# Kernel optimization log

Hardware: AMD Instinct MI355X
Metric: run time of the kernel (lower is better)

Reference implementation:

```python
import jax, jax.numpy as jnp
import numpy as np

N, E, MUL = 50000, 400000, 32
SQ3 = float(np.sqrt(3.0))


def setup_inputs() -> dict:
    key = jax.random.key(0)
    ks = jax.random.split(key, 16)
    rn = lambda k, s: jax.random.normal(k, s, dtype=jnp.float32)
    return {
        "x": rn(ks[0], (N, 4 * MUL)),                       # 32x0e + 32x1o
        "node_attr": jnp.ones((N, 1), jnp.float32),          # 1x0e
        "edge_src": jax.random.randint(ks[1], (E,), 0, N),
        "edge_dst": jax.random.randint(ks[2], (E,), 0, N),
        "edge_sh": rn(ks[3], (E, 4)),                        # SH(lmax=1): 0e + 1o
        "edge_scalars": jax.random.uniform(ks[4], (E, 10), dtype=jnp.float32),
        "W_fc1": rn(ks[5], (10, 100)),
        "W_fc2": rn(ks[6], (100, 4 * MUL)),
        "W_sc0": rn(ks[7], (MUL, MUL)),
        "W_sc1": rn(ks[8], (MUL, MUL)),
        "W_l1_0": rn(ks[9], (MUL, MUL)),
        "W_l1_1": rn(ks[10], (MUL, MUL)),
        "W_l2_0": rn(ks[11], (2 * MUL, MUL)),
        "W_l2_1": rn(ks[12], (2 * MUL, MUL)),
        "W_alpha": rn(ks[13], (2 * MUL, 1)),
    }


def reference(x, node_attr, edge_src, edge_dst, edge_sh, edge_scalars,
              W_fc1, W_fc2, W_sc0, W_sc1, W_l1_0, W_l1_1, W_l2_0, W_l2_1, W_alpha):
    n = x.shape[0]
    x0 = x[:, :MUL]                       # [N, 32]  scalars (0e)
    x1 = x[:, MUL:].reshape(n, MUL, 3)    # [N, 32, 3] vectors (1o)
    a = node_attr                          # [N, 1]
    inv = 1.0 / np.sqrt(MUL)
    inv2 = 1.0 / np.sqrt(2 * MUL)

    # self-connection FCTP(x, attr) -> out irreps (attr is scalar -> per-l linear)
    sc0 = (x0 @ W_sc0) * inv * a
    sc1 = jnp.einsum('nuc,uv->nvc', x1, W_sc1) * inv * a[:, :, None]
    sc = jnp.concatenate([sc0, sc1.reshape(n, 3 * MUL)], axis=1)

    # lin1
    y0 = (x0 @ W_l1_0) * inv * a
    y1 = jnp.einsum('nuc,uv->nvc', x1, W_l1_1) * inv * a[:, :, None]

    # radial MLP -> per-edge tensor-product weights (4 uvu paths x MUL)
    h = jax.nn.silu(edge_scalars @ W_fc1 / np.sqrt(10.0))
    w = (h @ W_fc2) / np.sqrt(100.0)      # [E, 4*MUL]
    w00, w11 = w[:, :MUL], w[:, MUL:2 * MUL]
    w01, w10 = w[:, 2 * MUL:3 * MUL], w[:, 3 * MUL:]

    # gather at source nodes
    x0e = y0[edge_src]                    # [E, 32]
    x1e = y1[edge_src]                    # [E, 32, 3]
    sh0 = edge_sh[:, :1]                  # [E, 1]
    sh1 = edge_sh[:, 1:4]                 # [E, 3]

    # CG-structured 'uvu' paths
    m00 = w00 * x0e * sh0                                           # 0e x 0e -> 0e
    m11 = w11 * jnp.einsum('euc,ec->eu', x1e, sh1) / SQ3            # 1o x 1o -> 0e
    m01 = w01[:, :, None] * x0e[:, :, None] * sh1[:, None, :]       # 0e x 1o -> 1o
    m10 = w10[:, :, None] * x1e * sh0[:, :, None]                   # 1o x 0e -> 1o
    edge_feat = jnp.concatenate(
        [m00, m11, m01.reshape(-1, 3 * MUL), m10.reshape(-1, 3 * MUL)], axis=1)  # [E, 256]

    # scatter-mean to destination nodes
    sums = jax.ops.segment_sum(edge_feat, edge_dst, num_segments=n)
    cnt = jax.ops.segment_sum(jnp.ones((edge_feat.shape[0],), x.dtype), edge_dst, num_segments=n)
    mean = sums / jnp.maximum(cnt, 1.0)[:, None]                    # [N, 256]

    mid0 = mean[:, :2 * MUL]                                        # 64x0e
    mid1 = mean[:, 2 * MUL:].reshape(n, 2 * MUL, 3)                 # 64x1o

    alpha = (mid0 @ W_alpha) * inv2 * a                             # [N, 1]
    c0 = (mid0 @ W_l2_0) * inv2 * a
    c1 = jnp.einsum('nuc,uv->nvc', mid1, W_l2_1) * inv2 * a[:, :, None]
    conv = jnp.concatenate([c0, c1.reshape(n, 3 * MUL)], axis=1)

    # output mask of sc is all ones here -> alpha gating as in source
    return sc + alpha * conv
```

## Files before the change

kernel.cpp:

```cpp
#include <hip/hip_runtime.h>
#include <hip/hip_bf16.h>

#define MUL 32
#define SCAN_CH 1024

typedef _Float16 f16x8 __attribute__((ext_vector_type(8)));
typedef float f32x4 __attribute__((ext_vector_type(4)));

static __device__ __forceinline__ float silu_f(float z) {
    return z / (1.0f + __expf(-z));
}

__global__ __launch_bounds__(256) void node_pre_kernel(
    const float* __restrict__ x, const float* __restrict__ attr,
    const float* __restrict__ Wsc0, const float* __restrict__ Wsc1,
    const float* __restrict__ Wl10, const float* __restrict__ Wl11,
    float* __restrict__ sc_out, _Float16* __restrict__ y_out, int N)
{
    __shared__ float sX[4][128];
    const int tid = threadIdx.x;
    const int wid = tid >> 6, L = tid & 63;
    float* xs = sX[wid];
    const float inv = 0.17677669529663687f;

    const bool t0 = (L < 32);
    const int i1 = t0 ? 0 : (L - 32);
    const int v1 = i1 / 3, c1 = i1 - v1 * 3;
    const int i2 = L + 32;
    const int v2 = i2 / 3, c2 = i2 - v2 * 3;

    const int xb1 = t0 ? 0 : (32 + c1);
    const int xst1 = t0 ? 1 : 3;

    float wA[32], wB[32], wC[32], wD[32];
#pragma unroll
    for (int u = 0; u < 32; ++u) {
        wA[u] = t0 ? Wsc0[u * 32 + L] : Wsc1[u * 32 + v1];
        wB[u] = t0 ? Wl10[u * 32 + L] : Wl11[u * 32 + v1];
        wC[u] = Wsc1[u * 32 + v2];
        wD[u] = Wl11[u * 32 + v2];
    }

    const int stride = gridDim.x * 4;
    for (int n = blockIdx.x * 4 + wid; n < N; n += stride) {
        xs[L]      = x[(size_t)n * 128 + L];
        xs[64 + L] = x[(size_t)n * 128 + 64 + L];
        const float scale = inv * attr[n];
        float a0 = 0.f, a1 = 0.f, b0 = 0.f, b1 = 0.f;
#pragma unroll
        for (int u = 0; u < 32; ++u) {
            const float xv1 = xs[xb1 + u * xst1];
            const float xv2 = xs[32 + u * 3 + c2];
            a0 += xv1 * wA[u];
            a1 += xv1 * wB[u];
            b0 += xv2 * wC[u];
            b1 += xv2 * wD[u];
        }
        sc_out[(size_t)n * 128 + L]      = a0 * scale;
        sc_out[(size_t)n * 128 + 64 + L] = b0 * scale;
        y_out [(size_t)n * 128 + L]      = (_Float16)(a1 * scale);
        y_out [(size_t)n * 128 + 64 + L] = (_Float16)(b1 * scale);
    }
}

__global__ void hist_kernel(const int* __restrict__ edst, int* __restrict__ deg, int E)
{
    int i = blockIdx.x * blockDim.x + threadIdx.x;
    const int stride = gridDim.x * blockDim.x;
    for (; i < E; i += stride) atomicAdd(&deg[edst[i]], 1);
}

__global__ __launch_bounds__(256) void scanA_kernel(
    const int* __restrict__ deg, int* __restrict__ bsum, int N)
{
    __shared__ int red[256];
    const int t = threadIdx.x, b = blockIdx.x;
    const int base = b * SCAN_CH;
    int s = 0;
#pragma unroll
    for (int k = 0; k < 4; ++k) {
        const int idx = base + t + k * 256;
        if (idx < N) s += deg[idx];
    }
    red[t] = s;
    __syncthreads();
    for (int off = 128; off; off >>= 1) {
        if (t < off) red[t] += red[t + off];
        __syncthreads();
    }
    if (t == 0) bsum[b] = red[0];
}

__global__ __launch_bounds__(256) void scanB_kernel(
    const int* __restrict__ bsum, int* __restrict__ boff, int NB)
{
    __shared__ int s[256];
    const int t = threadIdx.x;
    const int v = (t < NB) ? bsum[t] : 0;
    s[t] = v;
    __syncthreads();
    for (int off = 1; off < 256; off <<= 1) {
        const int add = (t >= off) ? s[t - off] : 0;
        __syncthreads();
        s[t] += add;
        __syncthreads();
    }
    if (t < NB) boff[t] = s[t] - v;
}

__global__ __launch_bounds__(256) void scanC_kernel(
    const int* __restrict__ deg, const int* __restrict__ boff,
    int* __restrict__ row_ptr, int N)
{
    __shared__ int ts[256];
    const int t = threadIdx.x, b = blockIdx.x;
    const int base = b * SCAN_CH + t * 4;
    int d0 = 0, d1 = 0, d2 = 0, d3 = 0;
    if (base + 0 < N) d0 = deg[base + 0];
    if (base + 1 < N) d1 = deg[base + 1];
    if (base + 2 < N) d2 = deg[base + 2];
    if (base + 3 < N) d3 = deg[base + 3];
    const int tsum = d0 + d1 + d2 + d3;
    ts[t] = tsum;
    __syncthreads();
    for (int off = 1; off < 256; off <<= 1) {
        const int add = (t >= off) ? ts[t - off] : 0;
        __syncthreads();
        ts[t] += add;
        __syncthreads();
    }
    int run = boff[b] + ts[t] - tsum;
    if (base + 0 <= N) row_ptr[base + 0] = run;
    run += d0;
    if (base + 1 <= N) row_ptr[base + 1] = run;
    run += d1;
    if (base + 2 <= N) row_ptr[base + 2] = run;
    run += d2;
    if (base + 3 <= N) row_ptr[base + 3] = run;
}

__global__ void fill_kernel(
    const int* __restrict__ esrc, const int* __restrict__ edst,
    const float* __restrict__ esh,
    const int* __restrict__ row_ptr, int* __restrict__ cur,
    int* __restrict__ csr2edge, int* __restrict__ src_s, float4* __restrict__ sh_s,
    int E)
{
    int i = blockIdx.x * blockDim.x + threadIdx.x;
    const int stride = gridDim.x * blockDim.x;
    for (; i < E; i += stride) {
        const int d = edst[i];
        const int p = row_ptr[d] + atomicAdd(&cur[d], 1);
        csr2edge[p] = i;
        src_s[p] = esrc[i];
        sh_s[p] = *(const float4*)&esh[(size_t)i * 4];
    }
}

__global__ __launch_bounds__(512) void edge_w_kernel(
    const float* __restrict__ escal, const int* __restrict__ csr2edge,
    const float* __restrict__ Wfc1, const float* __restrict__ Wfc2,
    _Float16* __restrict__ w_s, int E)
{
    __shared__ _Float16 sW2T[128 * 128];
    __shared__ _Float16 sH[8][16 * 128];

    const int tid = threadIdx.x;
    const int wid = tid >> 6;
    const int l   = tid & 63;
    const int c16 = l & 15;
    const int kq  = l >> 4;

    _Float16* Hw = sH[wid];

    {
        int* z2 = (int*)sW2T;
        for (int i = tid; i < 128 * 128 / 2; i += 512) z2[i] = 0;
    }
    __syncthreads();
    for (int i = tid; i < 100 * 128; i += 512) {
        const int k = i >> 7, col = i & 127;
        sW2T[col * 128 + (k ^ ((col & 7) << 3))] = (_Float16)Wfc2[i];
    }

    f16x8 bW1[7];
#pragma unroll
    for (int cb = 0; cb < 7; ++cb) {
        const int col = cb * 16 + c16;
#pragma unroll
        for (int j = 0; j < 8; ++j) {
            const int k = kq * 8 + j;
            bW1[cb][j] = (k < 10 && col < 100) ? (_Float16)Wfc1[k * 100 + col]
                                               : (_Float16)0.f;
        }
    }
#pragma unroll
    for (int r = 0; r < 4; ++r) {
        const int row = kq * 4 + r;
        const int col = 112 + c16;
        Hw[row * 128 + (col ^ ((row & 7) << 3))] = (_Float16)0.f;
    }
    __syncthreads();

    const float inv_s10 = 0.31622776601683794f;

    const int gw = blockIdx.x * 8 + wid;
    const int nw = gridDim.x * 8;
    const int step = nw * 16;

    int base = gw * 16;
    f16x8 a1;
    {
        const int ge = base + c16;
        const int ee = (ge < E) ? csr2edge[ge] : 0;
#pragma unroll
        for (int j = 0; j < 8; ++j) {
            const int k = kq * 8 + j;
            a1[j] = (k < 10 && ge < E) ? (_Float16)escal[(size_t)ee * 10 + k]
                                       : (_Float16)0.f;
        }
    }

    for (; base < E; base += step) {
#pragma unroll
        for (int cb = 0; cb < 7; ++cb) {
            f32x4 z = {0.f, 0.f, 0.f, 0.f};
            z = __builtin_amdgcn_mfma_f32_16x16x32_f16(a1, bW1[cb], z, 0, 0, 0);
#pragma unroll
            for (int r = 0; r < 4; ++r) {
                const int row = kq * 4 + r;
                const int col = cb * 16 + c16;
                const float h = silu_f(z[r] * inv_s10) * 0.1f;
                Hw[row * 128 + (col ^ ((row & 7) << 3))] = (_Float16)h;
            }
        }

        f16x8 a1n;
        {
            const int ge = base + step + c16;
            const int ee = (ge < E) ? csr2edge[ge] : 0;
#pragma unroll
            for (int j = 0; j < 8; ++j) {
                const int k = kq * 8 + j;
                a1n[j] = (k < 10 && ge < E)
                         ? (_Float16)escal[(size_t)ee * 10 + k]
                         : (_Float16)0.f;
            }
        }

        f32x4 acc0 = {0.f,0.f,0.f,0.f}, acc1 = {0.f,0.f,0.f,0.f};
        f32x4 acc2 = {0.f,0.f,0.f,0.f}, acc3 = {0.f,0.f,0.f,0.f};
        f32x4 acc4 = {0.f,0.f,0.f,0.f}, acc5 = {0.f,0.f,0.f,0.f};
        f32x4 acc6 = {0.f,0.f,0.f,0.f}, acc7 = {0.f,0.f,0.f,0.f};
#pragma unroll
        for (int kk = 0; kk < 4; ++kk) {
            const f16x8 a2 = *(const f16x8*)&Hw[c16 * 128 +
                                ((kk * 32 + kq * 8) ^ ((c16 & 7) << 3))];
#define BFRAG(CB) (*(const f16x8*)&sW2T[((CB) * 16 + c16) * 128 + \
                       ((kk * 32 + kq * 8) ^ ((c16 & 7) << 3))])
            acc0 = __builtin_amdgcn_mfma_f32_16x16x32_f16(a2, BFRAG(0), acc0, 0, 0, 0);
            acc1 = __builtin_amdgcn_mfma_f32_16x16x32_f16(a2, BFRAG(1), acc1, 0, 0, 0);
            acc2 = __builtin_amdgcn_mfma_f32_16x16x32_f16(a2, BFRAG(2), acc2, 0, 0, 0);
            acc3 = __builtin_amdgcn_mfma_f32_16x16x32_f16(a2, BFRAG(3), acc3, 0, 0, 0);
            acc4 = __builtin_amdgcn_mfma_f32_16x16x32_f16(a2, BFRAG(4), acc4, 0, 0, 0);
            acc5 = __builtin_amdgcn_mfma_f32_16x16x32_f16(a2, BFRAG(5), acc5, 0, 0, 0);
            acc6 = __builtin_amdgcn_mfma_f32_16x16x32_f16(a2, BFRAG(6), acc6, 0, 0, 0);
            acc7 = __builtin_amdgcn_mfma_f32_16x16x32_f16(a2, BFRAG(7), acc7, 0, 0, 0);
#undef BFRAG
        }

#define STAGE_CB(CB, ACC)                                                     \
        {                                                                     \
            _Pragma("unroll")                                                 \
            for (int r = 0; r < 4; ++r) {                                     \
                const int row = kq * 4 + r;                                   \
                const int col = (CB) * 16 + c16;                              \
                Hw[row * 128 + (col ^ ((row & 7) << 3))] = (_Float16)(ACC)[r];\
            }                                                                 \
        }
        STAGE_CB(0, acc0) STAGE_CB(1, acc1) STAGE_CB(2, acc2) STAGE_CB(3, acc3)
        STAGE_CB(4, acc4) STAGE_CB(5, acc5) STAGE_CB(6, acc6) STAGE_CB(7, acc7)
#undef STAGE_CB

#pragma unroll
        for (int i = 0; i < 4; ++i) {
            const int e = i * 4 + (l >> 4);
            const int colb = (l & 15) * 8;
            const f16x8 v = *(const f16x8*)&Hw[e * 128 +
                                (colb ^ ((e & 7) << 3))];
            if (base + e < E)
                *(f16x8*)&w_s[(size_t)(base + e) * 128 + colb] = v;
        }

        a1 = a1n;
    }
}

__global__ __launch_bounds__(256) void gather_post_kernel(
    const _Float16* __restrict__ w_s, const int* __restrict__ src_s,
    const float4* __restrict__ sh_s, const int* __restrict__ row_ptr,
    const _Float16* __restrict__ y, const float* __restrict__ attr,
    const float* __restrict__ Wl20, const float* __restrict__ Wl21,
    const float* __restrict__ Walpha,
    float* __restrict__ out, int N)
{
    __shared__ float sW0T[32 * 68];
    __shared__ float sW1T[32 * 68];
    __shared__ float sWa[64];
    __shared__ float sMid[4][256];

    const int tid = threadIdx.x;
    for (int i = tid; i < 64 * 32; i += 256) {
        const int u = i >> 5, o = i & 31;
        sW0T[o * 68 + u] = Wl20[i];
        sW1T[o * 68 + u] = Wl21[i];
    }
    if (tid < 64) sWa[tid] = Walpha[tid];
    __syncthreads();

    const int wid = tid >> 6;
    const int L   = tid & 63;
    const bool hi = (L >= 32);
    const int u   = L & 31;

    const int wAi = hi ? 32 + u : u;
    const int wBi = hi ? 96 + u : 64 + u;
    const int yi0 = hi ? 32 + 3 * u + 0 : u;
    const int yi1 = hi ? 32 + 3 * u + 1 : u;
    const int yi2 = hi ? 32 + 3 * u + 2 : u;
    const float mulA = hi ? 0.5773502691896258f : 1.0f;

    const int o1m = L - 32;
    const int v1 = hi ? o1m / 3 : 0;
    const int c1 = hi ? o1m - v1 * 3 : 0;
    const int o2m = L + 32;
    const int v2 = o2m / 3;
    const int c2 = o2m - v2 * 3;
    const float* wrow1 = hi ? (sW1T + v1 * 68) : (sW0T + L * 68);
    const float* wrow2 = sW1T + v2 * 68;

    float* midw = &sMid[wid][0];
    const float* msrc1c = hi ? (midw + 64 + c1 * 64) : midw;
    const float* msrc2c = midw + 64 + c2 * 64;

#define ACC_EDGE(sh, wAv, wBv, q0, q1, q2) do {                        \
        const float sA0 = hi ? (sh).y : (sh).x;                        \
        const float sA1 = hi ? (sh).z : 0.f;                           \
        const float sA2 = hi ? (sh).w : 0.f;                           \
        const float b1s = hi ? (sh).x : (sh).y;                        \
        const float b2s = hi ? (sh).x : (sh).z;                        \
        const float b3s = hi ? (sh).x : (sh).w;                        \
        accA += (wAv) * mulA * ((q0) * sA0 + (q1) * sA1 + (q2) * sA2); \
        acc1 += (wBv) * (q0) * b1s;                                    \
        acc2 += (wBv) * (q1) * b2s;                                    \
        acc3 += (wBv) * (q2) * b3s;                                    \
    } while (0)

    const int waves_glob = gridDim.x * 4;
    for (int n = blockIdx.x * 4 + wid; n < N; n += waves_glob) {
        const int jlo = row_ptr[n];
        const int jhi = row_ptr[n + 1];
        const int deg = jhi - jlo;
        if (deg <= 0) continue;

        float accA = 0.f, acc1 = 0.f, acc2 = 0.f, acc3 = 0.f;

        int j = jlo;
        for (; j + 2 <= jhi; j += 2) {
            const int sa = src_s[j];
            const int sb = src_s[j + 1];
            const float4 shA = sh_s[j];
            const float4 shB = sh_s[j + 1];
            const _Float16* wra = w_s + (size_t)j * 128;
            const _Float16* wrb = wra + 128;
            const _Float16* yra = y + (size_t)sa * 128;
            const _Float16* yrb = y + (size_t)sb * 128;
            const float wAa = (float)wra[wAi], wBa = (float)wra[wBi];
            const float qa0 = (float)yra[yi0], qa1 = (float)yra[yi1], qa2 = (float)yra[yi2];
            const float wAb = (float)wrb[wAi], wBb = (float)wrb[wBi];
            const float qb0 = (float)yrb[yi0], qb1 = (float)yrb[yi1], qb2 = (float)yrb[yi2];
            ACC_EDGE(shA, wAa, wBa, qa0, qa1, qa2);
            ACC_EDGE(shB, wAb, wBb, qb0, qb1, qb2);
        }
        if (j < jhi) {
            const int sa = src_s[j];
            const float4 shA = sh_s[j];
            const _Float16* wra = w_s + (size_t)j * 128;
            const _Float16* yra = y + (size_t)sa * 128;
            const float wAa = (float)wra[wAi], wBa = (float)wra[wBi];
            const float qa0 = (float)yra[yi0], qa1 = (float)yra[yi1], qa2 = (float)yra[yi2];
            ACC_EDGE(shA, wAa, wBa, qa0, qa1, qa2);
        }

        const float rdeg = 1.0f / (float)deg;
        const float a = attr[n];

        float term = accA * rdeg * sWa[L];
#pragma unroll
        for (int off = 32; off; off >>= 1) term += __shfl_xor(term, off);
        const float alpha = term * 0.125f * a;

        midw[L]            = accA * rdeg;
        midw[64 + L]       = acc1 * rdeg;
        midw[128 + L]      = acc2 * rdeg;
        midw[192 + L]      = acc3 * rdeg;

        float cv1 = 0.f, cv2 = 0.f;
#pragma unroll
        for (int kk = 0; kk < 16; ++kk) {
            const float4 m1 = *(const float4*)&msrc1c[4 * kk];
            const float4 m2 = *(const float4*)&msrc2c[4 * kk];
            const float4 w1 = *(const float4*)&wrow1[4 * kk];
            const float4 w2 = *(const float4*)&wrow2[4 * kk];
            cv1 += m1.x * w1.x + m1.y * w1.y + m1.z * w1.z + m1.w * w1.w;
            cv2 += m2.x * w2.x + m2.y * w2.y + m2.z * w2.z + m2.w * w2.w;
        }
        const float f = alpha * 0.125f * a;
        const size_t ob = (size_t)n * 128;
        out[ob + L]      += f * cv1;
        out[ob + 64 + L] += f * cv2;
    }
#undef ACC_EDGE
}

extern "C" void kernel_launch(void* const* d_in, const int* in_sizes, int n_in,
                              void* d_out, int out_size, void* d_ws, size_t ws_size,
                              hipStream_t stream)
{
    const float* x      = (const float*)d_in[0];
    const float* attr   = (const float*)d_in[1];
    const int*   esrc   = (const int*)  d_in[2];
    const int*   edst   = (const int*)  d_in[3];
    const float* esh    = (const float*)d_in[4];
    const float* escal  = (const float*)d_in[5];
    const float* Wfc1   = (const float*)d_in[6];
    const float* Wfc2   = (const float*)d_in[7];
    const float* Wsc0   = (const float*)d_in[8];
    const float* Wsc1   = (const float*)d_in[9];
    const float* Wl10   = (const float*)d_in[10];
    const float* Wl11   = (const float*)d_in[11];
    const float* Wl20   = (const float*)d_in[12];
    const float* Wl21   = (const float*)d_in[13];
    const float* Walpha = (const float*)d_in[14];

    const int N = in_sizes[1];
    const int E = in_sizes[2];
    float* out = (float*)d_out;

    char* p = (char*)d_ws;
    _Float16* y   = (_Float16*)p; p += (size_t)N * 128 * sizeof(_Float16);
    int* row_ptr  = (int*)p;      p += (size_t)(N + 1) * sizeof(int);
    int* deg      = (int*)p;      p += (size_t)N * sizeof(int);
    int* cur      = (int*)p;      p += (size_t)N * sizeof(int);
    int* bsum     = (int*)p;      p += 256 * sizeof(int);
    int* boff     = (int*)p;      p += 256 * sizeof(int);
    int* csr2edge = (int*)p;      p += (size_t)E * sizeof(int);
    int* src_s    = (int*)p;      p += (size_t)E * sizeof(int);
    p = (char*)(((uintptr_t)p + 15) & ~(uintptr_t)15);
    float4* sh_s  = (float4*)p;   p += (size_t)E * sizeof(float4);
    _Float16* w_s = (_Float16*)p;

    const int NB = (N + SCAN_CH) / SCAN_CH;

    hipMemsetAsync(deg, 0, (size_t)2 * N * sizeof(int), stream);

    node_pre_kernel<<<1024, 256, 0, stream>>>(x, attr, Wsc0, Wsc1, Wl10, Wl11,
                                              out, y, N);
    hist_kernel<<<512, 256, 0, stream>>>(edst, deg, E);
    scanA_kernel<<<NB, 256, 0, stream>>>(deg, bsum, N);
    scanB_kernel<<<1, 256, 0, stream>>>(bsum, boff, NB);
    scanC_kernel<<<NB, 256, 0, stream>>>(deg, boff, row_ptr, N);
    fill_kernel<<<512, 256, 0, stream>>>(esrc, edst, esh, row_ptr, cur,
                                         csr2edge, src_s, sh_s, E);
    edge_w_kernel<<<512, 512, 0, stream>>>(escal, csr2edge, Wfc1, Wfc2, w_s, E);
    gather_post_kernel<<<4096, 256, 0, stream>>>(w_s, src_s, sh_s, row_ptr,
                                                 y, attr, Wl20, Wl21, Walpha,
                                                 out, N);
}
```

Measured before the change: 237.0 us.

## Double-buffer per-wave H tile in edge weight MLP and halve block size

Restructures the edge radial-MLP kernel so each wave keeps two LDS H buffers and runs a software pipeline: the second GEMM and store of the current tile are followed by the first GEMM plus SiLU of the next tile, with escal loads prefetched two steps ahead. The block shrinks from 8 waves to 4 to keep LDS use the same, which halves the total number of waves in the 512-block grid. This aims to overlap MFMA, LDS traffic and global loads within a wave, but fewer waves means less latency hiding across waves.

```diff
diff --git a/kernel.cpp b/kernel.cpp
--- a/kernel.cpp
+++ b/kernel.cpp
@@ -157,13 +157,13 @@
     }
 }
 
-__global__ __launch_bounds__(512) void edge_w_kernel(
+__global__ __launch_bounds__(256) void edge_w_kernel(
     const float* __restrict__ escal, const int* __restrict__ csr2edge,
     const float* __restrict__ Wfc1, const float* __restrict__ Wfc2,
     _Float16* __restrict__ w_s, int E)
 {
     __shared__ _Float16 sW2T[128 * 128];
-    __shared__ _Float16 sH[8][16 * 128];
+    __shared__ _Float16 sH[4][2][16 * 128];
 
     const int tid = threadIdx.x;
     const int wid = tid >> 6;
@@ -171,14 +171,15 @@
     const int c16 = l & 15;
     const int kq  = l >> 4;
 
-    _Float16* Hw = sH[wid];
+    _Float16* Hw0 = sH[wid][0];
+    _Float16* Hw1 = sH[wid][1];
 
     {
         int* z2 = (int*)sW2T;
-        for (int i = tid; i < 128 * 128 / 2; i += 512) z2[i] = 0;
-    }
-    __syncthreads();
-    for (int i = tid; i < 100 * 128; i += 512) {
+        for (int i = tid; i < 128 * 128 / 2; i += 256) z2[i] = 0;
+    }
+    __syncthreads();
+    for (int i = tid; i < 100 * 128; i += 256) {
         const int k = i >> 7, col = i & 127;
         sW2T[col * 128 + (k ^ ((col & 7) << 3))] = (_Float16)Wfc2[i];
     }
@@ -198,102 +199,118 @@
     for (int r = 0; r < 4; ++r) {
         const int row = kq * 4 + r;
         const int col = 112 + c16;
-        Hw[row * 128 + (col ^ ((row & 7) << 3))] = (_Float16)0.f;
+        Hw0[row * 128 + (col ^ ((row & 7) << 3))] = (_Float16)0.f;
+        Hw1[row * 128 + (col ^ ((row & 7) << 3))] = (_Float16)0.f;
     }
     __syncthreads();
 
     const float inv_s10 = 0.31622776601683794f;
 
-    const int gw = blockIdx.x * 8 + wid;
-    const int nw = gridDim.x * 8;
+    const int gw = blockIdx.x * 4 + wid;
+    const int nw = gridDim.x * 4;
     const int step = nw * 16;
 
-    int base = gw * 16;
-    f16x8 a1;
-    {
-        const int ge = base + c16;
-        const int ee = (ge < E) ? csr2edge[ge] : 0;
-#pragma unroll
-        for (int j = 0; j < 8; ++j) {
-            const int k = kq * 8 + j;
-            a1[j] = (k < 10 && ge < E) ? (_Float16)escal[(size_t)ee * 10 + k]
-                                       : (_Float16)0.f;
-        }
-    }
-
-    for (; base < E; base += step) {
-#pragma unroll
-        for (int cb = 0; cb < 7; ++cb) {
-            f32x4 z = {0.f, 0.f, 0.f, 0.f};
-            z = __builtin_amdgcn_mfma_f32_16x16x32_f16(a1, bW1[cb], z, 0, 0, 0);
-#pragma unroll
-            for (int r = 0; r < 4; ++r) {
-                const int row = kq * 4 + r;
-                const int col = cb * 16 + c16;
-                const float h = silu_f(z[r] * inv_s10) * 0.1f;
-                Hw[row * 128 + (col ^ ((row & 7) << 3))] = (_Float16)h;
-            }
-        }
-
-        f16x8 a1n;
-        {
-            const int ge = base + step + c16;
-            const int ee = (ge < E) ? csr2edge[ge] : 0;
-#pragma unroll
-            for (int j = 0; j < 8; ++j) {
-                const int k = kq * 8 + j;
-                a1n[j] = (k < 10 && ge < E)
-                         ? (_Float16)escal[(size_t)ee * 10 + k]
-                         : (_Float16)0.f;
-            }
-        }
-
-        f32x4 acc0 = {0.f,0.f,0.f,0.f}, acc1 = {0.f,0.f,0.f,0.f};
-        f32x4 acc2 = {0.f,0.f,0.f,0.f}, acc3 = {0.f,0.f,0.f,0.f};
-        f32x4 acc4 = {0.f,0.f,0.f,0.f}, acc5 = {0.f,0.f,0.f,0.f};
-        f32x4 acc6 = {0.f,0.f,0.f,0.f}, acc7 = {0.f,0.f,0.f,0.f};
-#pragma unroll
-        for (int kk = 0; kk < 4; ++kk) {
-            const f16x8 a2 = *(const f16x8*)&Hw[c16 * 128 +
-                                ((kk * 32 + kq * 8) ^ ((c16 & 7) << 3))];
-#define BFRAG(CB) (*(const f16x8*)&sW2T[((CB) * 16 + c16) * 128 + \
-                       ((kk * 32 + kq * 8) ^ ((c16 & 7) << 3))])
-            acc0 = __builtin_amdgcn_mfma_f32_16x16x32_f16(a2, BFRAG(0), acc0, 0, 0, 0);
-            acc1 = __builtin_amdgcn_mfma_f32_16x16x32_f16(a2, BFRAG(1), acc1, 0, 0, 0);
-            acc2 = __builtin_amdgcn_mfma_f32_16x16x32_f16(a2, BFRAG(2), acc2, 0, 0, 0);
-            acc3 = __builtin_amdgcn_mfma_f32_16x16x32_f16(a2, BFRAG(3), acc3, 0, 0, 0);
-            acc4 = __builtin_amdgcn_mfma_f32_16x16x32_f16(a2, BFRAG(4), acc4, 0, 0, 0);
-            acc5 = __builtin_amdgcn_mfma_f32_16x16x32_f16(a2, BFRAG(5), acc5, 0, 0, 0);
-            acc6 = __builtin_amdgcn_mfma_f32_16x16x32_f16(a2, BFRAG(6), acc6, 0, 0, 0);
-            acc7 = __builtin_amdgcn_mfma_f32_16x16x32_f16(a2, BFRAG(7), acc7, 0, 0, 0);
-#undef BFRAG
-        }
-
-#define STAGE_CB(CB, ACC)                                                     \
+#define LOAD_A1(DST, B)                                                       \
+    {                                                                         \
+        const int ge_ = (B) + c16;                                            \
+        const int ee_ = (ge_ < E) ? csr2edge[ge_] : 0;                        \
+        _Pragma("unroll")                                                     \
+        for (int j_ = 0; j_ < 8; ++j_) {                                      \
+            const int k_ = kq * 8 + j_;                                       \
+            (DST)[j_] = (k_ < 10 && ge_ < E)                                  \
+                        ? (_Float16)escal[(size_t)ee_ * 10 + k_]              \
+                        : (_Float16)0.f;                                      \
+        }                                                                     \
+    }
+
+#define PHASE1(A1, H)                                                         \
+    {                                                                         \
+        _Pragma("unroll")                                                     \
+        for (int cb_ = 0; cb_ < 7; ++cb_) {                                   \
+            f32x4 z_ = {0.f, 0.f, 0.f, 0.f};                                  \
+            z_ = __builtin_amdgcn_mfma_f32_16x16x32_f16((A1), bW1[cb_], z_, 0, 0, 0); \
+            _Pragma("unroll")                                                 \
+            for (int r_ = 0; r_ < 4; ++r_) {                                  \
+                const int row_ = kq * 4 + r_;                                 \
+                const int col_ = cb_ * 16 + c16;                              \
+                const float h_ = silu_f(z_[r_] * inv_s10) * 0.1f;             \
+                (H)[row_ * 128 + (col_ ^ ((row_ & 7) << 3))] = (_Float16)h_;  \
+            }                                                                 \
+        }                                                                     \
+    }
+
+#define PHASE2_STORE(H, B)                                                    \
+    {                                                                         \
+        f32x4 ac0 = {0.f,0.f,0.f,0.f}, ac1 = {0.f,0.f,0.f,0.f};               \
+        f32x4 ac2 = {0.f,0.f,0.f,0.f}, ac3 = {0.f,0.f,0.f,0.f};               \
+        f32x4 ac4 = {0.f,0.f,0.f,0.f}, ac5 = {0.f,0.f,0.f,0.f};               \
+        f32x4 ac6 = {0.f,0.f,0.f,0.f}, ac7 = {0.f,0.f,0.f,0.f};               \
+        _Pragma("unroll")                                                     \
+        for (int kk_ = 0; kk_ < 4; ++kk_) {                                   \
+            const f16x8 a2_ = *(const f16x8*)&(H)[c16 * 128 +                 \
+                                ((kk_ * 32 + kq * 8) ^ ((c16 & 7) << 3))];    \
+            ac0 = __builtin_amdgcn_mfma_f32_16x16x32_f16(a2_, BFRAG(0, kk_), ac0, 0, 0, 0); \
+            ac1 = __builtin_amdgcn_mfma_f32_16x16x32_f16(a2_, BFRAG(1, kk_), ac1, 0, 0, 0); \
+            ac2 = __builtin_amdgcn_mfma_f32_16x16x32_f16(a2_, BFRAG(2, kk_), ac2, 0, 0, 0); \
+            ac3 = __builtin_amdgcn_mfma_f32_16x16x32_f16(a2_, BFRAG(3, kk_), ac3, 0, 0, 0); \
+            ac4 = __builtin_amdgcn_mfma_f32_16x16x32_f16(a2_, BFRAG(4, kk_), ac4, 0, 0, 0); \
+            ac5 = __builtin_amdgcn_mfma_f32_16x16x32_f16(a2_, BFRAG(5, kk_), ac5, 0, 0, 0); \
+            ac6 = __builtin_amdgcn_mfma_f32_16x16x32_f16(a2_, BFRAG(6, kk_), ac6, 0, 0, 0); \
+            ac7 = __builtin_amdgcn_mfma_f32_16x16x32_f16(a2_, BFRAG(7, kk_), ac7, 0, 0, 0); \
+        }                                                                     \
+        STAGE_CB((H), 0, ac0) STAGE_CB((H), 1, ac1)                           \
+        STAGE_CB((H), 2, ac2) STAGE_CB((H), 3, ac3)                           \
+        STAGE_CB((H), 4, ac4) STAGE_CB((H), 5, ac5)                           \
+        STAGE_CB((H), 6, ac6) STAGE_CB((H), 7, ac7)                           \
+        _Pragma("unroll")                                                     \
+        for (int i_ = 0; i_ < 4; ++i_) {                                      \
+            const int e_ = i_ * 4 + (l >> 4);                                 \
+            const int colb_ = (l & 15) * 8;                                   \
+            const f16x8 v_ = *(const f16x8*)&(H)[e_ * 128 +                   \
+                                (colb_ ^ ((e_ & 7) << 3))];                   \
+            if ((B) + e_ < E)                                                 \
+                *(f16x8*)&w_s[(size_t)((B) + e_) * 128 + colb_] = v_;         \
+        }                                                                     \
+    }
+
+#define BFRAG(CB, KK) (*(const f16x8*)&sW2T[((CB) * 16 + c16) * 128 + \
+                           (((KK) * 32 + kq * 8) ^ ((c16 & 7) << 3))])
+#define STAGE_CB(H, CB, ACC)                                                  \
         {                                                                     \
             _Pragma("unroll")                                                 \
-            for (int r = 0; r < 4; ++r) {                                     \
-                const int row = kq * 4 + r;                                   \
-                const int col = (CB) * 16 + c16;                              \
-                Hw[row * 128 + (col ^ ((row & 7) << 3))] = (_Float16)(ACC)[r];\
+            for (int r_ = 0; r_ < 4; ++r_) {                                  \
+                const int row_ = kq * 4 + r_;                                 \
+                const int col_ = (CB) * 16 + c16;                             \
+                (H)[row_ * 128 + (col_ ^ ((row_ & 7) << 3))] = (_Float16)(ACC)[r_]; \
             }                                                                 \
         }
-        STAGE_CB(0, acc0) STAGE_CB(1, acc1) STAGE_CB(2, acc2) STAGE_CB(3, acc3)
-        STAGE_CB(4, acc4) STAGE_CB(5, acc5) STAGE_CB(6, acc6) STAGE_CB(7, acc7)
+
+    int base = gw * 16;
+    if (base >= E) return;
+
+    f16x8 a1;
+    LOAD_A1(a1, base)
+    PHASE1(a1, Hw0)
+    LOAD_A1(a1, base + step)
+
+    int par = 0;
+    for (; base + step < E; base += step, par ^= 1) {
+        _Float16* Hc = par ? Hw1 : Hw0;
+        _Float16* Hn = par ? Hw0 : Hw1;
+        PHASE2_STORE(Hc, base)
+        PHASE1(a1, Hn)
+        LOAD_A1(a1, base + 2 * step)
+    }
+    {
+        _Float16* Hc = par ? Hw1 : Hw0;
+        PHASE2_STORE(Hc, base)
+    }
+
+#undef LOAD_A1
+#undef PHASE1
+#undef PHASE2_STORE
+#undef BFRAG
 #undef STAGE_CB
-
-#pragma unroll
-        for (int i = 0; i < 4; ++i) {
-            const int e = i * 4 + (l >> 4);
-            const int colb = (l & 15) * 8;
-            const f16x8 v = *(const f16x8*)&Hw[e * 128 +
-                                (colb ^ ((e & 7) << 3))];
-            if (base + e < E)
-                *(f16x8*)&w_s[(size_t)(base + e) * 128 + colb] = v;
-        }
-
-        a1 = a1n;
-    }
 }
 
 __global__ __launch_bounds__(256) void gather_post_kernel(
@@ -472,7 +489,7 @@
     scanC_kernel<<<NB, 256, 0, stream>>>(deg, boff, row_ptr, N);
     fill_kernel<<<512, 256, 0, stream>>>(esrc, edst, esh, row_ptr, cur,
                                          csr2edge, src_s, sh_s, E);
-    edge_w_kernel<<<512, 512, 0, stream>>>(escal, csr2edge, Wfc1, Wfc2, w_s, E);
+    edge_w_kernel<<<512, 256, 0, stream>>>(escal, csr2edge, Wfc1, Wfc2, w_s, E);
     gather_post_kernel<<<4096, 256, 0, stream>>>(w_s, src_s, sh_s, row_ptr,
                                                  y, attr, Wl20, Wl21, Walpha,
                                                  out, N);
```

After: 270.1 us. 14.0% more time.
